# Performance work log

Hardware: AMD Instinct MI355X
Metric: run time of the kernel (lower is better)

## Reference

```python
import jax, jax.numpy as jnp
import numpy as np

B, J = 131072, 24
# SMPL skeleton parent indices (root = joint 0)
SMPL_PARENTS = np.array([-1, 0, 0, 0, 1, 2, 3, 4, 5, 6, 7, 8, 9, 9, 9, 12, 13, 14, 16, 17, 18, 19, 20, 21], dtype=np.int64)


def setup_inputs() -> dict:
    key = jax.random.key(0)
    k1, k2 = jax.random.split(key)
    positions = jax.random.normal(k1, (B, J, 3), dtype=jnp.float32)
    rotations = jax.random.normal(k2, (B, J, 4), dtype=jnp.float32)
    return {"parents": SMPL_PARENTS, "positions": positions, "rotations": rotations}


def _quat_to_rotmat(q):
    # q: [B, J, 4] (w, x, y, z); normalize then standard unit-quaternion rotation matrix
    q = q / jnp.linalg.norm(q, axis=-1, keepdims=True)
    qw, qx, qy, qz = q[..., 0], q[..., 1], q[..., 2], q[..., 3]
    x2, y2, z2 = qx + qx, qy + qy, qz + qz
    xx, yy, zz = qx * x2, qy * y2, qz * z2
    xy, yz, xz = qx * y2, qy * z2, qx * z2
    wx, wy, wz = qw * x2, qw * y2, qw * z2
    row0 = jnp.stack([1.0 - (yy + zz), xy - wz, xz + wy], axis=-1)
    row1 = jnp.stack([xy + wz, 1.0 - (xx + zz), yz - wx], axis=-1)
    row2 = jnp.stack([xz - wy, yz + wx, 1.0 - (xx + yy)], axis=-1)
    return jnp.stack([row0, row1, row2], axis=-2)  # [B, J, 3, 3]


def _local_transforms(positions, rotations):
    R = _quat_to_rotmat(rotations)                       # [B, J, 3, 3]
    top = jnp.concatenate([R, positions[..., None]], axis=-1)  # [B, J, 3, 4]
    bottom = jnp.broadcast_to(
        jnp.array([0.0, 0.0, 0.0, 1.0], dtype=rotations.dtype), top.shape[:2] + (1, 4))
    return jnp.concatenate([top, bottom], axis=-2)       # [B, J, 4, 4]


def reference(parents, positions, rotations):
    parents = np.asarray(parents)  # static skeleton topology
    locals_ = _local_transforms(positions, rotations)    # [B, J, 4, 4]
    n_joints = parents.shape[0]
    # Sequential parent-child chain over the (small, static) joint tree.
    g = [locals_[:, 0]]
    for jt in range(1, n_joints):
        g.append(jnp.matmul(g[int(parents[jt])], locals_[:, jt]))
    globals_ = jnp.stack(g, axis=1)                      # [B, J, 4, 4]
    p = globals_[:, :, :, 3]                             # homogeneous positions [B, J, 4]
    return p[:, :, :3] / p[:, :, 3:4]                    # [B, J, 3]
```

## Files before the change

### kernel.cpp

```cpp
#include <hip/hip_runtime.h>


typedef float f32x4 __attribute__((ext_vector_type(4)));

struct M { float r0,r1,r2,r3,r4,r5,r6,r7,r8,tx,ty,tz; };

__device__ __forceinline__ M loc(float a, float b, float c, float d,
                                 float px, float py, float pz) {
    float inv = rsqrtf(a*a + b*b + c*c + d*d);
    float qw = a*inv, qx = b*inv, qy = c*inv, qz = d*inv;
    float x2 = qx+qx, y2 = qy+qy, z2 = qz+qz;
    float xx = qx*x2, yy = qy*y2, zz = qz*z2;
    float xy = qx*y2, yz = qy*z2, xz = qx*z2;
    float wx = qw*x2, wy = qw*y2, wz = qw*z2;
    M m;
    m.r0 = 1.f-(yy+zz); m.r1 = xy-wz;       m.r2 = xz+wy;
    m.r3 = xy+wz;       m.r4 = 1.f-(xx+zz); m.r5 = yz-wx;
    m.r6 = xz-wy;       m.r7 = yz+wx;       m.r8 = 1.f-(xx+yy);
    m.tx = px; m.ty = py; m.tz = pz;
    return m;
}

__device__ __forceinline__ M mul(const M& a, const M& b) {
    M c;
    c.r0 = a.r0*b.r0 + a.r1*b.r3 + a.r2*b.r6;
    c.r1 = a.r0*b.r1 + a.r1*b.r4 + a.r2*b.r7;
    c.r2 = a.r0*b.r2 + a.r1*b.r5 + a.r2*b.r8;
    c.r3 = a.r3*b.r0 + a.r4*b.r3 + a.r5*b.r6;
    c.r4 = a.r3*b.r1 + a.r4*b.r4 + a.r5*b.r7;
    c.r5 = a.r3*b.r2 + a.r4*b.r5 + a.r5*b.r8;
    c.r6 = a.r6*b.r0 + a.r7*b.r3 + a.r8*b.r6;
    c.r7 = a.r6*b.r1 + a.r7*b.r4 + a.r8*b.r7;
    c.r8 = a.r6*b.r2 + a.r7*b.r5 + a.r8*b.r8;
    c.tx = a.r0*b.tx + a.r1*b.ty + a.r2*b.tz + a.tx;
    c.ty = a.r3*b.tx + a.r4*b.ty + a.r5*b.tz + a.ty;
    c.tz = a.r6*b.tx + a.r7*b.ty + a.r8*b.tz + a.tz;
    return c;
}

#define SPB    64
#define NTHR   512
#define GRIDP  256
#define RPITCH 100
#define PPITCH 73

constexpr int MT0[6]  = {0,1,2,4,7,10};
constexpr int PR0[6]  = {-1,0,0,1,3,4};
constexpr int MT1[8]  = {0,2,5,8,11,3,6,9};
constexpr int PR1[8]  = {-1,0,1,2,3,0,5,6};
constexpr int MT2[11] = {0,3,6,9,12,15,13,16,18,20,22};
constexpr int PR2[11] = {-1,0,1,2,3,4,3,6,7,8,9};
constexpr int MT3[9]  = {0,3,6,9,14,17,19,21,23};
constexpr int PR3[9]  = {-1,0,1,2,3,4,5,6,7};

template<int NM>
__device__ __forceinline__ void run_chain(const int (&MT)[NM], const int (&PR)[NM],
                                          int WS,
                                          const float* __restrict__ R,
                                          const float* __restrict__ P,
                                          float* __restrict__ O) {
    M G[NM];
    {
        f32x4 q = *(const f32x4*)(R);
        G[0] = loc(q.x, q.y, q.z, q.w, P[0], P[1], P[2]);
    }
    if (WS == 0) { O[0]=G[0].tx; O[1]=G[0].ty; O[2]=G[0].tz; }
#pragma unroll
    for (int k = 1; k < NM; ++k) {
        const int j = MT[k];
        f32x4 q = *(const f32x4*)(R + 4*j);
        M L = loc(q.x, q.y, q.z, q.w, P[3*j], P[3*j+1], P[3*j+2]);
        G[k] = mul(G[PR[k]], L);
        if (k >= WS) { O[3*j]=G[k].tx; O[3*j+1]=G[k].ty; O[3*j+2]=G[k].tz; }
    }
}

__device__ __forceinline__ void load_regs(int c, int mt,
                                          const float* __restrict__ rot,
                                          const float* __restrict__ pos,
                                          size_t limR, size_t limP,
                                          f32x4 (&vr)[6], f32x4 (&vp)[5]) {
    const size_t baseR = (size_t)c * (SPB*96);
    const size_t baseP = (size_t)c * (SPB*72);
#pragma unroll
    for (int i = 0; i < 6; ++i) {
        const size_t gi = baseR + (size_t)(i*1024 + 4*mt);
        f32x4 v = {0.f,0.f,0.f,0.f};
        if (gi < limR) v = *(const f32x4*)(rot + gi);
        vr[i] = v;
    }
#pragma unroll
    for (int i = 0; i < 5; ++i) {
        const bool g = (i < 4) || (mt < 128);
        const size_t gi = baseP + (size_t)(i*1024 + 4*mt);
        f32x4 v = {0.f,0.f,0.f,0.f};
        if (g && gi < limP) v = *(const f32x4*)(pos + gi);
        vp[i] = v;
    }
}

__device__ __forceinline__ void scatter_lds(int mt,
                                            float* __restrict__ Rb,
                                            float* __restrict__ Pb,
                                            const f32x4 (&vr)[6],
                                            const f32x4 (&vp)[5]) {
#pragma unroll
    for (int i = 0; i < 6; ++i) {
        const int f = i*1024 + 4*mt;
        const int s = f / 96, r = f - 96*s;
        *(f32x4*)(Rb + s*RPITCH + r) = vr[i];
    }
#pragma unroll
    for (int i = 0; i < 5; ++i) {
        if ((i < 4) || (mt < 128)) {
            const int f = i*1024 + 4*mt;
            const int s = f / 72, r = f - 72*s;
            float* d = Pb + s*PPITCH + r;
            d[0]=vp[i].x; d[1]=vp[i].y; d[2]=vp[i].z; d[3]=vp[i].w;
        }
    }
}

__device__ __forceinline__ void store_chunk(const float* __restrict__ Ob,
                                            int c, int mt, size_t limP,
                                            float* __restrict__ out) {
    const size_t baseO = (size_t)c * (SPB*72);
#pragma unroll
    for (int n = 0; n < 5; ++n) {
        if ((n < 4) || (mt < 128)) {
            const int F = n*1024 + 4*mt;
            const int s = F / 72, r = F - 72*s;
            const size_t gi = baseO + (size_t)F;
            if (gi < limP) {
                f32x4 v = { Ob[s*PPITCH+r+0], Ob[s*PPITCH+r+1],
                            Ob[s*PPITCH+r+2], Ob[s*PPITCH+r+3] };
                __builtin_nontemporal_store(v, (f32x4*)(out + gi));
            }
        }
    }
}

__global__ __launch_bounds__(NTHR, 2) void fk_kernel(
    const float* __restrict__ rot,
    const float* __restrict__ pos,
    float*       __restrict__ out,
    int B)
{
    __shared__ __align__(16) float ldsR[2][SPB * RPITCH];
    __shared__ float ldsP[2][SPB * PPITCH];
    __shared__ float ldsO[2][SPB * PPITCH];

    const int t   = threadIdx.x;
    const int w   = t >> 6;
    const bool cw = (w < 4);
    const int mt  = t & 255;
    const int nch = (B + SPB - 1) / SPB;
    const size_t limR = (size_t)B * 96;
    const size_t limP = (size_t)B * 72;

    const int c0 = blockIdx.x;
    if (!cw && c0 < nch) {
        f32x4 vr[6], vp[5];
        load_regs(c0, mt, rot, pos, limR, limP, vr, vp);
        scatter_lds(mt, ldsR[0], ldsP[0], vr, vp);
    }
    __syncthreads();

    int i = 0, c = c0;
    for (; c < nch; c += GRIDP, ++i) {
        const int q = i & 1;
        if (cw) {
            const int l = t & 63;
            const int b = c * SPB + l;
            if (b < B) {
                const float* R = &ldsR[q][l * RPITCH];
                const float* P = &ldsP[q][l * PPITCH];
                float*       O = &ldsO[q][l * PPITCH];
                switch (w) {
                    case 0:  run_chain(MT0, PR0, 0, R, P, O); break;
                    case 1:  run_chain(MT1, PR1, 2, R, P, O); break;
                    case 2:  run_chain(MT2, PR2, 4, R, P, O); break;
                    default: run_chain(MT3, PR3, 4, R, P, O); break;
                }
            }
        } else {
            const int cn = c + GRIDP;
            const bool ldv = (cn < nch);
            f32x4 vr[6], vp[5];
            if (ldv) load_regs(cn, mt, rot, pos, limR, limP, vr, vp);
            if (i > 0) store_chunk(ldsO[q^1], c - GRIDP, mt, limP, out);
            if (ldv) scatter_lds(mt, ldsR[q^1], ldsP[q^1], vr, vp);
        }
        __syncthreads();
    }

    if (!cw && i > 0)
        store_chunk(ldsO[(i-1) & 1], c - GRIDP, mt, limP, out);
}

extern "C" void kernel_launch(void* const* d_in, const int* in_sizes, int n_in,
                              void* d_out, int out_size, void* d_ws, size_t ws_size,
                              hipStream_t stream) {
    const int B = out_size / 72;
    const void* rot = nullptr;
    const void* pos = nullptr;
    for (int i = 0; i < n_in; ++i) {
        if      (in_sizes[i] == B * 96) rot = d_in[i];
        else if (in_sizes[i] == B * 72) pos = d_in[i];
    }
    if (!rot) rot = d_in[2];
    if (!pos) pos = d_in[1];

    const int nch  = (B + SPB - 1) / SPB;
    const int grid = (nch < GRIDP) ? nch : GRIDP;
    fk_kernel<<<grid, NTHR, 0, stream>>>(
        (const float*)rot, (const float*)pos, (float*)d_out, B);
}
```

Measured before the change: 124.0 us.

## Drop output LDS buffer, reuse rotation buffer, shrink chunks for higher occupancy

```diff
diff --git a/kernel.cpp b/kernel.cpp
--- a/kernel.cpp
+++ b/kernel.cpp
@@ -38,11 +38,12 @@
     return c;
 }
 
-#define SPB    64
+#define SPB    56
 #define NTHR   512
-#define GRIDP  256
+#define GRIDP  512
 #define RPITCH 100
 #define PPITCH 73
+#define OPITCH 73
 
 constexpr int MT0[6]  = {0,1,2,4,7,10};
 constexpr int PR0[6]  = {-1,0,0,1,3,4};
@@ -58,20 +59,36 @@
                                           int WS,
                                           const float* __restrict__ R,
                                           const float* __restrict__ P,
-                                          float* __restrict__ O) {
+                                          float* __restrict__ ob) {
     M G[NM];
     {
         f32x4 q = *(const f32x4*)(R);
         G[0] = loc(q.x, q.y, q.z, q.w, P[0], P[1], P[2]);
     }
-    if (WS == 0) { O[0]=G[0].tx; O[1]=G[0].ty; O[2]=G[0].tz; }
+    if (WS == 0) { ob[0]=G[0].tx; ob[1]=G[0].ty; ob[2]=G[0].tz; }
 #pragma unroll
     for (int k = 1; k < NM; ++k) {
         const int j = MT[k];
         f32x4 q = *(const f32x4*)(R + 4*j);
         M L = loc(q.x, q.y, q.z, q.w, P[3*j], P[3*j+1], P[3*j+2]);
         G[k] = mul(G[PR[k]], L);
-        if (k >= WS) { O[3*j]=G[k].tx; O[3*j+1]=G[k].ty; O[3*j+2]=G[k].tz; }
+        if (k >= WS) {
+            const int o = 3*(k-WS);
+            ob[o+0]=G[k].tx; ob[o+1]=G[k].ty; ob[o+2]=G[k].tz;
+        }
+    }
+}
+
+template<int NM>
+__device__ __forceinline__ void emit_out(const int (&MT)[NM], int WS,
+                                         const float* __restrict__ ob,
+                                         float* __restrict__ ovl) {
+#pragma unroll
+    for (int k = 0; k < NM; ++k) {
+        if (k >= WS) {
+            const int j = MT[k], o = 3*(k-WS);
+            ovl[3*j+0]=ob[o+0]; ovl[3*j+1]=ob[o+1]; ovl[3*j+2]=ob[o+2];
+        }
     }
 }
 
@@ -79,19 +96,20 @@
                                           const float* __restrict__ rot,
                                           const float* __restrict__ pos,
                                           size_t limR, size_t limP,
-                                          f32x4 (&vr)[6], f32x4 (&vp)[5]) {
+                                          f32x4 (&vr)[6], f32x4 (&vp)[4]) {
     const size_t baseR = (size_t)c * (SPB*96);
     const size_t baseP = (size_t)c * (SPB*72);
 #pragma unroll
     for (int i = 0; i < 6; ++i) {
+        const bool g = (i < 5) || (mt < 64);
         const size_t gi = baseR + (size_t)(i*1024 + 4*mt);
         f32x4 v = {0.f,0.f,0.f,0.f};
-        if (gi < limR) v = *(const f32x4*)(rot + gi);
+        if (g && gi < limR) v = *(const f32x4*)(rot + gi);
         vr[i] = v;
     }
 #pragma unroll
-    for (int i = 0; i < 5; ++i) {
-        const bool g = (i < 4) || (mt < 128);
+    for (int i = 0; i < 4; ++i) {
+        const bool g = (i < 3) || (mt < 240);
         const size_t gi = baseP + (size_t)(i*1024 + 4*mt);
         f32x4 v = {0.f,0.f,0.f,0.f};
         if (g && gi < limP) v = *(const f32x4*)(pos + gi);
@@ -100,19 +118,21 @@
 }
 
 __device__ __forceinline__ void scatter_lds(int mt,
-                                            float* __restrict__ Rb,
-                                            float* __restrict__ Pb,
+                                            float* Rb,
+                                            float* Pb,
                                             const f32x4 (&vr)[6],
-                                            const f32x4 (&vp)[5]) {
+                                            const f32x4 (&vp)[4]) {
 #pragma unroll
     for (int i = 0; i < 6; ++i) {
-        const int f = i*1024 + 4*mt;
-        const int s = f / 96, r = f - 96*s;
-        *(f32x4*)(Rb + s*RPITCH + r) = vr[i];
-    }
-#pragma unroll
-    for (int i = 0; i < 5; ++i) {
-        if ((i < 4) || (mt < 128)) {
+        if ((i < 5) || (mt < 64)) {
+            const int f = i*1024 + 4*mt;
+            const int s = f / 96, r = f - 96*s;
+            *(f32x4*)(Rb + s*RPITCH + r) = vr[i];
+        }
+    }
+#pragma unroll
+    for (int i = 0; i < 4; ++i) {
+        if ((i < 3) || (mt < 240)) {
             const int f = i*1024 + 4*mt;
             const int s = f / 72, r = f - 72*s;
             float* d = Pb + s*PPITCH + r;
@@ -121,26 +141,26 @@
     }
 }
 
-__device__ __forceinline__ void store_chunk(const float* __restrict__ Ob,
+__device__ __forceinline__ void store_chunk(const float* Ov,
                                             int c, int mt, size_t limP,
                                             float* __restrict__ out) {
     const size_t baseO = (size_t)c * (SPB*72);
 #pragma unroll
-    for (int n = 0; n < 5; ++n) {
-        if ((n < 4) || (mt < 128)) {
+    for (int n = 0; n < 4; ++n) {
+        if ((n < 3) || (mt < 240)) {
             const int F = n*1024 + 4*mt;
             const int s = F / 72, r = F - 72*s;
             const size_t gi = baseO + (size_t)F;
             if (gi < limP) {
-                f32x4 v = { Ob[s*PPITCH+r+0], Ob[s*PPITCH+r+1],
-                            Ob[s*PPITCH+r+2], Ob[s*PPITCH+r+3] };
+                f32x4 v = { Ov[s*OPITCH+r+0], Ov[s*OPITCH+r+1],
+                            Ov[s*OPITCH+r+2], Ov[s*OPITCH+r+3] };
                 __builtin_nontemporal_store(v, (f32x4*)(out + gi));
             }
         }
     }
 }
 
-__global__ __launch_bounds__(NTHR, 2) void fk_kernel(
+__global__ __launch_bounds__(NTHR, 4) void fk_kernel(
     const float* __restrict__ rot,
     const float* __restrict__ pos,
     float*       __restrict__ out,
@@ -148,7 +168,6 @@
 {
     __shared__ __align__(16) float ldsR[2][SPB * RPITCH];
     __shared__ float ldsP[2][SPB * PPITCH];
-    __shared__ float ldsO[2][SPB * PPITCH];
 
     const int t   = threadIdx.x;
     const int w   = t >> 6;
@@ -159,43 +178,60 @@
     const size_t limP = (size_t)B * 72;
 
     const int c0 = blockIdx.x;
-    if (!cw && c0 < nch) {
-        f32x4 vr[6], vp[5];
-        load_regs(c0, mt, rot, pos, limR, limP, vr, vp);
-        scatter_lds(mt, ldsR[0], ldsP[0], vr, vp);
+    {
+        f32x4 vr[6]; f32x4 vp[4];
+        if (!cw && c0 < nch) {
+            load_regs(c0, mt, rot, pos, limR, limP, vr, vp);
+            scatter_lds(mt, ldsR[0], ldsP[0], vr, vp);
+        }
     }
     __syncthreads();
 
     int i = 0, c = c0;
+    float ob[21];
+    f32x4 vr[6]; f32x4 vp[4];
     for (; c < nch; c += GRIDP, ++i) {
         const int q = i & 1;
+        const int l = t & 63;
+        const bool ldv = (c + GRIDP) < nch;
+
         if (cw) {
-            const int l = t & 63;
             const int b = c * SPB + l;
-            if (b < B) {
+            if ((l < SPB) && (b < B)) {
                 const float* R = &ldsR[q][l * RPITCH];
                 const float* P = &ldsP[q][l * PPITCH];
-                float*       O = &ldsO[q][l * PPITCH];
                 switch (w) {
-                    case 0:  run_chain(MT0, PR0, 0, R, P, O); break;
-                    case 1:  run_chain(MT1, PR1, 2, R, P, O); break;
-                    case 2:  run_chain(MT2, PR2, 4, R, P, O); break;
-                    default: run_chain(MT3, PR3, 4, R, P, O); break;
+                    case 0:  run_chain(MT0, PR0, 0, R, P, ob); break;
+                    case 1:  run_chain(MT1, PR1, 2, R, P, ob); break;
+                    case 2:  run_chain(MT2, PR2, 4, R, P, ob); break;
+                    default: run_chain(MT3, PR3, 4, R, P, ob); break;
                 }
             }
         } else {
-            const int cn = c + GRIDP;
-            const bool ldv = (cn < nch);
-            f32x4 vr[6], vp[5];
-            if (ldv) load_regs(cn, mt, rot, pos, limR, limP, vr, vp);
-            if (i > 0) store_chunk(ldsO[q^1], c - GRIDP, mt, limP, out);
+            if (ldv) load_regs(c + GRIDP, mt, rot, pos, limR, limP, vr, vp);
+            if (i > 0) store_chunk(&ldsR[q^1][0], c - GRIDP, mt, limP, out);
+        }
+        __syncthreads();
+
+        if (cw) {
+            const int b = c * SPB + l;
+            if ((l < SPB) && (b < B)) {
+                float* ovl = &ldsR[q][l * OPITCH];
+                switch (w) {
+                    case 0:  emit_out(MT0, 0, ob, ovl); break;
+                    case 1:  emit_out(MT1, 2, ob, ovl); break;
+                    case 2:  emit_out(MT2, 4, ob, ovl); break;
+                    default: emit_out(MT3, 4, ob, ovl); break;
+                }
+            }
+        } else {
             if (ldv) scatter_lds(mt, ldsR[q^1], ldsP[q^1], vr, vp);
         }
         __syncthreads();
     }
 
     if (!cw && i > 0)
-        store_chunk(ldsO[(i-1) & 1], c - GRIDP, mt, limP, out);
+        store_chunk(&ldsR[(i-1) & 1][0], c - GRIDP, mt, limP, out);
 }
 
 extern "C" void kernel_launch(void* const* d_in, const int* in_sizes, int n_in,
```

Result: slower. 184.9 us (+49.2%).
